# Performance work log

Hardware: AMD Instinct MI355X
Metric: run time of the kernel (lower is better)

Reference implementation:

```python
import jax, jax.numpy as jnp
import numpy as np

N_NODES = 100000   # users + items
EMB_DIM = 64
N_EDGES = 3200000  # avg degree 32
N_LAYERS = 3


def setup_inputs() -> dict:
    key = jax.random.key(0)
    k1, k2, k3, k4 = jax.random.split(key, 4)
    emb = jax.random.normal(k1, (N_NODES, EMB_DIM), dtype=jnp.float32)
    rows = jax.random.randint(k2, (N_EDGES,), 0, N_NODES, dtype=jnp.int32)
    cols = jax.random.randint(k3, (N_EDGES,), 0, N_NODES, dtype=jnp.int32)
    vals = jax.random.uniform(k4, (N_EDGES,), dtype=jnp.float32)
    return {"ItemAndUserEmebddings": emb, "adj_rows": rows,
            "adj_cols": cols, "adj_vals": vals}


def _spmm(rows, cols, vals, x):
    # (sparse A) @ x : gather source rows, scale by edge value, scatter-add to dest
    msgs = vals[:, None] * x[cols]                      # [E, d]
    return jax.ops.segment_sum(msgs, rows, num_segments=x.shape[0])


def reference(ItemAndUserEmebddings, adj_rows, adj_cols, adj_vals):
    all_emb = ItemAndUserEmebddings
    embeddings_list = [all_emb]
    for _ in range(N_LAYERS):
        all_emb = _spmm(adj_rows, adj_cols, adj_vals, all_emb)
        embeddings_list.append(all_emb)
    stacked = jnp.stack(embeddings_list, axis=1)        # [N, L+1, d]
    lightgcn_all_embeddings = jnp.mean(stacked, axis=1)  # [N, d]
    return (lightgcn_all_embeddings, stacked)
```

## Files before the change

kernel.cpp:

```cpp
#include <hip/hip_runtime.h>
#include <hip/hip_fp16.h>

#define N_NODES 100000
#define EMB_DIM 64
#define N_EDGES 3200000
#define N_LAYERS 3

#define SCAN_BLOCK 512
#define N_SCAN_BLOCKS ((N_NODES + SCAN_BLOCK - 1) / SCAN_BLOCK)

#define ABINROWS 256
#define NBINS ((N_NODES + ABINROWS - 1) / ABINROWS)
#define NBINS_P 512
#define ACHUNK 2048
#define AEPT 8
#define NCHUNKS ((N_EDGES + ACHUNK - 1) / ACHUNK)


__device__ __forceinline__ unsigned short f32_to_bf16_rtn(float f) {
    unsigned u = __float_as_uint(f);
    unsigned r = u + 0x7FFFu + ((u >> 16) & 1u);
    return (unsigned short)(r >> 16);
}
__device__ __forceinline__ float bf16_to_f32(unsigned short h) {
    return __uint_as_float(((unsigned)h) << 16);
}


__global__ void count_rows(const int* __restrict__ rows, int* __restrict__ counts) {
    int e = blockIdx.x * blockDim.x + threadIdx.x;
    if (e >= N_EDGES) return;
    atomicAdd(&counts[rows[e]], 1);
}

__global__ void __launch_bounds__(SCAN_BLOCK) scan_phase1(const int* __restrict__ counts,
                                                          int* __restrict__ blockSums) {
    __shared__ int sm[SCAN_BLOCK];
    int idx = blockIdx.x * SCAN_BLOCK + threadIdx.x;
    int v = (idx < N_NODES) ? counts[idx] : 0;
    sm[threadIdx.x] = v;
    __syncthreads();
    for (int off = SCAN_BLOCK / 2; off > 0; off >>= 1) {
        if (threadIdx.x < off) sm[threadIdx.x] += sm[threadIdx.x + off];
        __syncthreads();
    }
    if (threadIdx.x == 0) blockSums[blockIdx.x] = sm[0];
}

__global__ void __launch_bounds__(256) scan_phase2(const int* __restrict__ blockSums,
                                                   int* __restrict__ blockOffs,
                                                   int* __restrict__ row_ptr) {
    __shared__ int sm[256];
    int t = threadIdx.x;
    int v = (t < N_SCAN_BLOCKS) ? blockSums[t] : 0;
    sm[t] = v;
    __syncthreads();
    for (int off = 1; off < 256; off <<= 1) {
        int u = (t >= off) ? sm[t - off] : 0;
        __syncthreads();
        sm[t] += u;
        __syncthreads();
    }
    if (t < N_SCAN_BLOCKS) blockOffs[t] = (t == 0) ? 0 : sm[t - 1];
    if (t == 255) row_ptr[N_NODES] = sm[255];
}

__global__ void __launch_bounds__(SCAN_BLOCK) scan_phase3(const int* __restrict__ counts,
                                                          const int* __restrict__ blockOffs,
                                                          int* __restrict__ row_ptr) {
    __shared__ int sm[SCAN_BLOCK];
    int idx = blockIdx.x * SCAN_BLOCK + threadIdx.x;
    int t = threadIdx.x;
    int v = (idx < N_NODES) ? counts[idx] : 0;
    sm[t] = v;
    __syncthreads();
    for (int off = 1; off < SCAN_BLOCK; off <<= 1) {
        int u = (t >= off) ? sm[t - off] : 0;
        __syncthreads();
        sm[t] += u;
        __syncthreads();
    }
    if (idx < N_NODES) row_ptr[idx] = blockOffs[blockIdx.x] + sm[t] - v;
}


__global__ void __launch_bounds__(256) build_sortA(const int* __restrict__ rows,
                                                   const int* __restrict__ cols,
                                                   const float* __restrict__ vals,
                                                   const int* __restrict__ row_ptr,
                                                   int* __restrict__ bucketFill,
                                                   uint2* __restrict__ records) {
    __shared__ int binCnt[NBINS_P];
    __shared__ int binInc[NBINS_P];
    __shared__ int binCur[NBINS_P];
    __shared__ int binG[NBINS];
    __shared__ uint2 buf[ACHUNK];

    int base = blockIdx.x * ACHUNK;
    int n = N_EDGES - base; if (n > ACHUNK) n = ACHUNK;
    int t = threadIdx.x;

    for (int i = t; i < NBINS_P; i += 256) { binCnt[i] = 0; binCur[i] = 0; }
    __syncthreads();

    int r_[AEPT]; unsigned pk_[AEPT];
#pragma unroll AEPT
    for (int k = 0; k < AEPT; ++k) {
        int i = t + k * 256;
        r_[k] = 0; pk_[k] = 0;
        if (i < n) {
            int e = base + i;
            int r = rows[e];
            unsigned hb = __half_as_ushort(__float2half(vals[e]));
            r_[k] = r;
            pk_[k] = (((unsigned)cols[e]) << 15) | (hb & 0x7FFFu);
            atomicAdd(&binCnt[r >> 8], 1);
        }
    }
    __syncthreads();

    binInc[t] = binCnt[t];
    binInc[t + 256] = binCnt[t + 256];
    __syncthreads();
    for (int off = 1; off < NBINS_P; off <<= 1) {
        int i0 = t, i1 = t + 256;
        int v0 = (i0 >= off) ? binInc[i0 - off] : 0;
        int v1 = (i1 >= off) ? binInc[i1 - off] : 0;
        __syncthreads();
        binInc[i0] += v0;
        binInc[i1] += v1;
        __syncthreads();
    }

#pragma unroll AEPT
    for (int k = 0; k < AEPT; ++k) {
        int i = t + k * 256;
        if (i < n) {
            int b = r_[k] >> 8;
            int slot = (binInc[b] - binCnt[b]) + atomicAdd(&binCur[b], 1);
            buf[slot] = make_uint2((unsigned)r_[k], pk_[k]);
        }
    }
    for (int b = t; b < NBINS; b += 256) {
        int c = binCnt[b];
        if (c > 0) binG[b] = row_ptr[b * ABINROWS] + atomicAdd(&bucketFill[b], c);
    }
    __syncthreads();

    for (int p = t; p < n; p += 256) {
        uint2 rec = buf[p];
        int b = (int)(rec.x >> 8);
        int dst = binG[b] + (p - (binInc[b] - binCnt[b]));
        records[dst] = rec;
    }
}

__global__ void __launch_bounds__(256) build_phaseB(const int* __restrict__ row_ptr,
                                                    const uint2* __restrict__ records,
                                                    unsigned* __restrict__ s_edges) {
    __shared__ int lfill[ABINROWS];
    __shared__ int lrp[ABINROWS];
    int b = blockIdx.x;
    int r0 = b * ABINROWS;
    int r1 = r0 + ABINROWS; if (r1 > N_NODES) r1 = N_NODES;
    int nr = r1 - r0;
    for (int i = threadIdx.x; i < nr; i += 256) { lfill[i] = 0; lrp[i] = row_ptr[r0 + i]; }
    __syncthreads();
    int beg = row_ptr[r0];
    int end = row_ptr[r1];
    for (int i = beg + threadIdx.x; i < end; i += 256) {
        uint2 rec = records[i];
        int lr = (int)rec.x - r0;
        int lp = atomicAdd(&lfill[lr], 1);
        s_edges[lrp[lr] + lp] = rec.y;
    }
}

__global__ void emb_to_bf16(const float* __restrict__ emb, ushort4* __restrict__ mirror) {
    int t = blockIdx.x * blockDim.x + threadIdx.x;
    if (t >= N_NODES * 16) return;
    float4 v = ((const float4*)emb)[t];
    ushort4 o;
    o.x = f32_to_bf16_rtn(v.x); o.y = f32_to_bf16_rtn(v.y);
    o.z = f32_to_bf16_rtn(v.z); o.w = f32_to_bf16_rtn(v.w);
    mirror[t] = o;
}


__device__ __forceinline__ void gacc(float4& acc, unsigned p, int j,
                                     const unsigned short* __restrict__ srcMirror) {
    float v = __half2float(__ushort_as_half((unsigned short)(p & 0x7FFFu)));
    ushort4 m = *(const ushort4*)(srcMirror + (size_t)(p >> 15) * 64 + j * 4);
    acc.x += v * bf16_to_f32(m.x);
    acc.y += v * bf16_to_f32(m.y);
    acc.z += v * bf16_to_f32(m.z);
    acc.w += v * bf16_to_f32(m.w);
}

__device__ __forceinline__ float4 spmm_row_core(int beg, int end, int g, int j, int lane,
                                                const unsigned* __restrict__ s_edges,
                                                const unsigned short* __restrict__ srcMirror) {
    int deg = end - beg;
    unsigned ew = (lane < deg) ? s_edges[beg + lane] : 0u;
    float4 acc = make_float4(0.f, 0.f, 0.f, 0.f);
    int nfull = deg < 64 ? deg : 64;
    for (int kb = 0; kb < nfull; kb += 16) {
        int k0 = kb + g, k1 = kb + g + 4, k2 = kb + g + 8, k3 = kb + g + 12;
        unsigned p0 = __shfl(ew, k0);
        unsigned p1 = __shfl(ew, k1);
        unsigned p2 = __shfl(ew, k2);
        unsigned p3 = __shfl(ew, k3);
        if (k0 < nfull) gacc(acc, p0, j, srcMirror);
        if (k1 < nfull) gacc(acc, p1, j, srcMirror);
        if (k2 < nfull) gacc(acc, p2, j, srcMirror);
        if (k3 < nfull) gacc(acc, p3, j, srcMirror);
    }
    for (int e = beg + 64 + g; e < end; e += 4) {
        unsigned p = s_edges[e];
        gacc(acc, p, j, srcMirror);
    }
    acc.x += __shfl_xor(acc.x, 16); acc.y += __shfl_xor(acc.y, 16);
    acc.z += __shfl_xor(acc.z, 16); acc.w += __shfl_xor(acc.w, 16);
    acc.x += __shfl_xor(acc.x, 32); acc.y += __shfl_xor(acc.y, 32);
    acc.z += __shfl_xor(acc.z, 32); acc.w += __shfl_xor(acc.w, 32);
    return acc;
}

__global__ void __launch_bounds__(256) spmm_gather_bf16_mid(const int* __restrict__ row_ptr,
                                                            const unsigned* __restrict__ s_edges,
                                                            const unsigned short* __restrict__ srcMirror,
                                                            float* __restrict__ dstStacked,
                                                            unsigned short* __restrict__ dstMirror) {
    int wave = (blockIdx.x * blockDim.x + threadIdx.x) >> 6;
    if (wave >= N_NODES) return;
    int lane = threadIdx.x & 63;
    int g = lane >> 4, j = lane & 15;
    float4 acc = spmm_row_core(row_ptr[wave], row_ptr[wave + 1], g, j, lane, s_edges, srcMirror);
    if (lane < 16) {
        *(float4*)(dstStacked + (size_t)wave * 256 + j * 4) = acc;
        ushort4 o;
        o.x = f32_to_bf16_rtn(acc.x); o.y = f32_to_bf16_rtn(acc.y);
        o.z = f32_to_bf16_rtn(acc.z); o.w = f32_to_bf16_rtn(acc.w);
        *(ushort4*)(dstMirror + (size_t)wave * 64 + j * 4) = o;
    }
}

__global__ void __launch_bounds__(256) spmm_gather_bf16_last(const int* __restrict__ row_ptr,
                                                             const unsigned* __restrict__ s_edges,
                                                             const unsigned short* __restrict__ srcMirror,
                                                             const float* __restrict__ emb,
                                                             float* __restrict__ stacked,
                                                             float* __restrict__ meanOut) {
    int wave = (blockIdx.x * blockDim.x + threadIdx.x) >> 6;
    if (wave >= N_NODES) return;
    int lane = threadIdx.x & 63;
    int g = lane >> 4, j = lane & 15;
    float4 acc = spmm_row_core(row_ptr[wave], row_ptr[wave + 1], g, j, lane, s_edges, srcMirror);
    if (lane < 16) {
        float4* base = (float4*)stacked + (size_t)wave * 64;
        float4 a = ((const float4*)emb)[wave * 16 + j];
        float4 b = base[16 + j];
        float4 c = base[32 + j];
        base[j] = a;
        base[48 + j] = acc;
        float4 s;
        s.x = 0.25f * (a.x + b.x + c.x + acc.x);
        s.y = 0.25f * (a.y + b.y + c.y + acc.y);
        s.z = 0.25f * (a.z + b.z + c.z + acc.z);
        s.w = 0.25f * (a.w + b.w + c.w + acc.w);
        ((float4*)meanOut)[wave * 16 + j] = s;
    }
}

__global__ void mean_layers(const float* __restrict__ emb,
                            float* __restrict__ stacked,
                            float* __restrict__ meanOut) {
    int t = blockIdx.x * blockDim.x + threadIdx.x;
    if (t >= N_NODES * 16) return;
    int n = t >> 4;
    int j = t & 15;
    float4* base = (float4*)stacked + (size_t)n * 64;
    float4 a = ((const float4*)emb)[t];
    float4 b = base[16 + j];
    float4 c = base[32 + j];
    float4 d = base[48 + j];
    base[j] = a;
    float4 s;
    s.x = 0.25f * (a.x + b.x + c.x + d.x);
    s.y = 0.25f * (a.y + b.y + c.y + d.y);
    s.z = 0.25f * (a.z + b.z + c.z + d.z);
    s.w = 0.25f * (a.w + b.w + c.w + d.w);
    ((float4*)meanOut)[t] = s;
}


__global__ void scatter_edges_int2(const int* __restrict__ rows, const int* __restrict__ cols,
                                   const float* __restrict__ vals,
                                   const int* __restrict__ row_ptr, int* __restrict__ fill,
                                   int2* __restrict__ s_colval) {
    int e = blockIdx.x * blockDim.x + threadIdx.x;
    if (e >= N_EDGES) return;
    int r = rows[e];
    int pos = row_ptr[r] + atomicAdd(&fill[r], 1);
    int2 p; p.x = cols[e]; p.y = __float_as_int(vals[e]);
    s_colval[pos] = p;
}

__global__ void __launch_bounds__(256) spmm_gather_f32(const int* __restrict__ row_ptr,
                                                       const int2* __restrict__ s_colval,
                                                       const float* __restrict__ src, int srcStride,
                                                       float* __restrict__ dst) {
    int wave = (blockIdx.x * blockDim.x + threadIdx.x) >> 6;
    if (wave >= N_NODES) return;
    int lane = threadIdx.x & 63;
    int g = lane >> 4, j = lane & 15;
    int beg = row_ptr[wave], end = row_ptr[wave + 1];
    float4 acc = make_float4(0.f, 0.f, 0.f, 0.f);
    int e = beg + g;
    for (; e + 4 < end; e += 8) {
        int2 p0 = s_colval[e], p1 = s_colval[e + 4];
        float v0 = __int_as_float(p0.y), v1 = __int_as_float(p1.y);
        float4 m0 = *(const float4*)(src + (size_t)p0.x * srcStride + j * 4);
        float4 m1 = *(const float4*)(src + (size_t)p1.x * srcStride + j * 4);
        acc.x += v0 * m0.x + v1 * m1.x; acc.y += v0 * m0.y + v1 * m1.y;
        acc.z += v0 * m0.z + v1 * m1.z; acc.w += v0 * m0.w + v1 * m1.w;
    }
    for (; e < end; e += 4) {
        int2 p = s_colval[e];
        float v = __int_as_float(p.y);
        float4 m = *(const float4*)(src + (size_t)p.x * srcStride + j * 4);
        acc.x += v * m.x; acc.y += v * m.y; acc.z += v * m.z; acc.w += v * m.w;
    }
    acc.x += __shfl_xor(acc.x, 16); acc.y += __shfl_xor(acc.y, 16);
    acc.z += __shfl_xor(acc.z, 16); acc.w += __shfl_xor(acc.w, 16);
    acc.x += __shfl_xor(acc.x, 32); acc.y += __shfl_xor(acc.y, 32);
    acc.z += __shfl_xor(acc.z, 32); acc.w += __shfl_xor(acc.w, 32);
    if (lane < 16)
        *(float4*)(dst + (size_t)wave * 256 + j * 4) = acc;
}


__global__ void init_stacked_full(const float* __restrict__ emb, float* __restrict__ stacked) {
    int t = blockIdx.x * blockDim.x + threadIdx.x;
    if (t >= N_NODES * 64) return;
    int n = t >> 6, j = t & 63;
    float4 v = (j < 16) ? ((const float4*)emb)[n * 16 + j] : make_float4(0.f, 0.f, 0.f, 0.f);
    ((float4*)stacked)[n * 64 + j] = v;
}

__global__ void spmm_atomic(const int* __restrict__ rows, const int* __restrict__ cols,
                            const float* __restrict__ vals, float* __restrict__ stacked,
                            int lprev) {
    int t = blockIdx.x * blockDim.x + threadIdx.x;
    int e = t >> 4, j = t & 15;
    if (e >= N_EDGES) return;
    int r = rows[e], c = cols[e];
    float v = vals[e];
    const float4* src = (const float4*)(stacked + (size_t)c * 256 + lprev * 64);
    float4 m = src[j];
    float* dst = stacked + (size_t)r * 256 + (lprev + 1) * 64 + j * 4;
    atomicAdd(dst + 0, v * m.x); atomicAdd(dst + 1, v * m.y);
    atomicAdd(dst + 2, v * m.z); atomicAdd(dst + 3, v * m.w);
}

__global__ void mean_layers_plain(const float* __restrict__ stacked, float* __restrict__ meanOut) {
    int t = blockIdx.x * blockDim.x + threadIdx.x;
    if (t >= N_NODES * 16) return;
    int n = t >> 4, j = t & 15;
    const float4* base = (const float4*)(stacked + (size_t)n * 256);
    float4 a = base[j], b = base[16 + j], c = base[32 + j], d = base[48 + j];
    float4 s;
    s.x = 0.25f * (a.x + b.x + c.x + d.x);
    s.y = 0.25f * (a.y + b.y + c.y + d.y);
    s.z = 0.25f * (a.z + b.z + c.z + d.z);
    s.w = 0.25f * (a.w + b.w + c.w + d.w);
    ((float4*)meanOut)[t] = s;
}

extern "C" void kernel_launch(void* const* d_in, const int* in_sizes, int n_in,
                              void* d_out, int out_size, void* d_ws, size_t ws_size,
                              hipStream_t stream) {
    const float* emb  = (const float*)d_in[0];
    const int*   rows = (const int*)d_in[1];
    const int*   cols = (const int*)d_in[2];
    const float* vals = (const float*)d_in[3];

    float* meanOut = (float*)d_out;
    float* stacked = (float*)d_out + (size_t)N_NODES * EMB_DIM;

    const size_t headInts = (size_t)(N_NODES * 2 + 1 + 2 * N_SCAN_BLOCKS);
    size_t need_bf16 = headInts * sizeof(int) + 64
                     + (size_t)N_EDGES * sizeof(unsigned)
                     + 2 * (size_t)N_NODES * EMB_DIM * sizeof(unsigned short);
    size_t need_f32  = headInts * sizeof(int) + 64 + (size_t)N_EDGES * sizeof(int2);

    if (ws_size >= need_bf16) {
        char* w = (char*)d_ws;
        int* counts    = (int*)w;  w += (size_t)N_NODES * sizeof(int);
        int* row_ptr   = (int*)w;  w += (size_t)(N_NODES + 1) * sizeof(int);
        int* blockSums = (int*)w;  w += (size_t)N_SCAN_BLOCKS * sizeof(int);
        int* blockOffs = (int*)w;  w += (size_t)N_SCAN_BLOCKS * sizeof(int);
        w = (char*)(((uintptr_t)w + 15) & ~(uintptr_t)15);
        unsigned* s_edges = (unsigned*)w;  w += (size_t)N_EDGES * sizeof(unsigned);
        unsigned short* mirrorA = (unsigned short*)w;  w += (size_t)N_NODES * EMB_DIM * sizeof(unsigned short);
        unsigned short* mirrorB = (unsigned short*)w;
        uint2* records = (uint2*)mirrorA;

        hipMemsetAsync(counts, 0, (size_t)N_NODES * sizeof(int), stream);
        {
            int block = 256, grid = (N_EDGES + block - 1) / block;
            count_rows<<<grid, block, 0, stream>>>(rows, counts);
        }
        scan_phase1<<<N_SCAN_BLOCKS, SCAN_BLOCK, 0, stream>>>(counts, blockSums);
        scan_phase2<<<1, 256, 0, stream>>>(blockSums, blockOffs, row_ptr);
        scan_phase3<<<N_SCAN_BLOCKS, SCAN_BLOCK, 0, stream>>>(counts, blockOffs, row_ptr);
        int* bucketFill = counts;
        hipMemsetAsync(bucketFill, 0, (size_t)NBINS * sizeof(int), stream);
        build_sortA<<<NCHUNKS, 256, 0, stream>>>(rows, cols, vals, row_ptr, bucketFill, records);
        build_phaseB<<<NBINS, 256, 0, stream>>>(row_ptr, records, s_edges);
        {
            int total = N_NODES * 16;
            int block = 256, grid = (total + block - 1) / block;
            emb_to_bf16<<<grid, block, 0, stream>>>(emb, (ushort4*)mirrorA);
        }
        {
            long long threads = (long long)N_NODES * 64;
            int block = 256;
            int grid = (int)((threads + block - 1) / block);
            spmm_gather_bf16_mid<<<grid, block, 0, stream>>>(row_ptr, s_edges, mirrorA, stacked + 1 * 64, mirrorB);
            spmm_gather_bf16_mid<<<grid, block, 0, stream>>>(row_ptr, s_edges, mirrorB, stacked + 2 * 64, mirrorA);
            spmm_gather_bf16_last<<<grid, block, 0, stream>>>(row_ptr, s_edges, mirrorA, emb, stacked, meanOut);
        }
    } else if (ws_size >= need_f32) {
        char* w = (char*)d_ws;
        int* counts    = (int*)w;  w += (size_t)N_NODES * sizeof(int);
        int* row_ptr   = (int*)w;  w += (size_t)(N_NODES + 1) * sizeof(int);
        int* blockSums = (int*)w;  w += (size_t)N_SCAN_BLOCKS * sizeof(int);
        int* blockOffs = (int*)w;  w += (size_t)N_SCAN_BLOCKS * sizeof(int);
        w = (char*)(((uintptr_t)w + 15) & ~(uintptr_t)15);
        int2* s_colval = (int2*)w;

        hipMemsetAsync(counts, 0, (size_t)N_NODES * sizeof(int), stream);
        {
            int block = 256, grid = (N_EDGES + block - 1) / block;
            count_rows<<<grid, block, 0, stream>>>(rows, counts);
        }
        scan_phase1<<<N_SCAN_BLOCKS, SCAN_BLOCK, 0, stream>>>(counts, blockSums);
        scan_phase2<<<1, 256, 0, stream>>>(blockSums, blockOffs, row_ptr);
        scan_phase3<<<N_SCAN_BLOCKS, SCAN_BLOCK, 0, stream>>>(counts, blockOffs, row_ptr);
        hipMemsetAsync(counts, 0, (size_t)N_NODES * sizeof(int), stream);
        {
            int block = 256, grid = (N_EDGES + block - 1) / block;
            scatter_edges_int2<<<grid, block, 0, stream>>>(rows, cols, vals, row_ptr, counts, s_colval);
        }
        {
            long long threads = (long long)N_NODES * 64;
            int block = 256;
            int grid = (int)((threads + block - 1) / block);
            spmm_gather_f32<<<grid, block, 0, stream>>>(row_ptr, s_colval, emb, 64, stacked + 1 * 64);
            spmm_gather_f32<<<grid, block, 0, stream>>>(row_ptr, s_colval, stacked + 1 * 64, 256, stacked + 2 * 64);
            spmm_gather_f32<<<grid, block, 0, stream>>>(row_ptr, s_colval, stacked + 2 * 64, 256, stacked + 3 * 64);
        }
        {
            int total = N_NODES * 16;
            int block = 256, grid = (total + block - 1) / block;
            mean_layers<<<grid, block, 0, stream>>>(emb, stacked, meanOut);
        }
    } else {
        {
            int total = N_NODES * 64;
            int block = 256, grid = (total + block - 1) / block;
            init_stacked_full<<<grid, block, 0, stream>>>(emb, stacked);
        }
        {
            long long total = (long long)N_EDGES * 16;
            int block = 256, grid = (int)((total + block - 1) / block);
            for (int l = 0; l < N_LAYERS; ++l)
                spmm_atomic<<<grid, block, 0, stream>>>(rows, cols, vals, stacked, l);
        }
        {
            int total = N_NODES * 16;
            int block = 256, grid = (total + block - 1) / block;
            mean_layers_plain<<<grid, block, 0, stream>>>(stacked, meanOut);
        }
    }
}
```

Before: 650.0 us.

## Build CSR row pointers from coarse bin histogram instead of per-row count+scan

```diff
diff --git a/kernel.cpp b/kernel.cpp
--- a/kernel.cpp
+++ b/kernel.cpp
@@ -15,6 +15,8 @@
 #define ACHUNK 2048
 #define AEPT 8
 #define NCHUNKS ((N_EDGES + ACHUNK - 1) / ACHUNK)
+#define BCHUNK 4096
+#define NBCHUNKS ((N_EDGES + BCHUNK - 1) / BCHUNK)
 
 
 __device__ __forceinline__ unsigned short f32_to_bf16_rtn(float f) {
@@ -24,6 +26,40 @@
 }
 __device__ __forceinline__ float bf16_to_f32(unsigned short h) {
     return __uint_as_float(((unsigned)h) << 16);
+}
+
+
+__global__ void __launch_bounds__(256) bin_count(const int* __restrict__ rows,
+                                                 int* __restrict__ binCounts) {
+    __shared__ int h[NBINS];
+    int t = threadIdx.x;
+    for (int i = t; i < NBINS; i += 256) h[i] = 0;
+    __syncthreads();
+    int base = blockIdx.x * BCHUNK;
+    int n = N_EDGES - base; if (n > BCHUNK) n = BCHUNK;
+    for (int i = t; i < n; i += 256) atomicAdd(&h[rows[base + i] >> 8], 1);
+    __syncthreads();
+    for (int i = t; i < NBINS; i += 256) {
+        int c = h[i];
+        if (c) atomicAdd(&binCounts[i], c);
+    }
+}
+
+__global__ void __launch_bounds__(512) bin_scan(const int* __restrict__ binCounts,
+                                                int* __restrict__ binPtr) {
+    __shared__ int sm[512];
+    int t = threadIdx.x;
+    int v = (t < NBINS) ? binCounts[t] : 0;
+    sm[t] = v;
+    __syncthreads();
+    for (int off = 1; off < 512; off <<= 1) {
+        int u = (t >= off) ? sm[t - off] : 0;
+        __syncthreads();
+        sm[t] += u;
+        __syncthreads();
+    }
+    if (t < NBINS) binPtr[t + 1] = sm[t];
+    if (t == 0) binPtr[0] = 0;
 }
 
 
@@ -87,7 +123,7 @@
 __global__ void __launch_bounds__(256) build_sortA(const int* __restrict__ rows,
                                                    const int* __restrict__ cols,
                                                    const float* __restrict__ vals,
-                                                   const int* __restrict__ row_ptr,
+                                                   const int* __restrict__ binPtr,
                                                    int* __restrict__ bucketFill,
                                                    uint2* __restrict__ records) {
     __shared__ int binCnt[NBINS_P];
@@ -143,7 +179,7 @@
     }
     for (int b = t; b < NBINS; b += 256) {
         int c = binCnt[b];
-        if (c > 0) binG[b] = row_ptr[b * ABINROWS] + atomicAdd(&bucketFill[b], c);
+        if (c > 0) binG[b] = binPtr[b] + atomicAdd(&bucketFill[b], c);
     }
     __syncthreads();
 
@@ -155,20 +191,41 @@
     }
 }
 
-__global__ void __launch_bounds__(256) build_phaseB(const int* __restrict__ row_ptr,
+__global__ void __launch_bounds__(256) build_phaseB(const int* __restrict__ binPtr,
                                                     const uint2* __restrict__ records,
-                                                    unsigned* __restrict__ s_edges) {
+                                                    unsigned* __restrict__ s_edges,
+                                                    int* __restrict__ row_ptr) {
+    __shared__ int lcnt[ABINROWS];
+    __shared__ int linc[ABINROWS];
+    __shared__ int lrp[ABINROWS];
     __shared__ int lfill[ABINROWS];
-    __shared__ int lrp[ABINROWS];
     int b = blockIdx.x;
+    int t = threadIdx.x;
     int r0 = b * ABINROWS;
     int r1 = r0 + ABINROWS; if (r1 > N_NODES) r1 = N_NODES;
     int nr = r1 - r0;
-    for (int i = threadIdx.x; i < nr; i += 256) { lfill[i] = 0; lrp[i] = row_ptr[r0 + i]; }
-    __syncthreads();
-    int beg = row_ptr[r0];
-    int end = row_ptr[r1];
-    for (int i = beg + threadIdx.x; i < end; i += 256) {
+    int beg = binPtr[b];
+    int end = binPtr[b + 1];
+
+    lcnt[t] = 0; lfill[t] = 0;
+    __syncthreads();
+    for (int i = beg + t; i < end; i += 256) {
+        atomicAdd(&lcnt[(int)records[i].x - r0], 1);
+    }
+    __syncthreads();
+    linc[t] = lcnt[t];
+    __syncthreads();
+    for (int off = 1; off < 256; off <<= 1) {
+        int u = (t >= off) ? linc[t - off] : 0;
+        __syncthreads();
+        linc[t] += u;
+        __syncthreads();
+    }
+    lrp[t] = beg + linc[t] - lcnt[t];
+    if (t < nr) row_ptr[r0 + t] = lrp[t];
+    if (t == 0) row_ptr[r0 + nr] = end;
+    __syncthreads();
+    for (int i = beg + t; i < end; i += 256) {
         uint2 rec = records[i];
         int lr = (int)rec.x - r0;
         int lp = atomicAdd(&lfill[lr], 1);
@@ -405,19 +462,15 @@
         unsigned short* mirrorA = (unsigned short*)w;  w += (size_t)N_NODES * EMB_DIM * sizeof(unsigned short);
         unsigned short* mirrorB = (unsigned short*)w;
         uint2* records = (uint2*)mirrorA;
-
-        hipMemsetAsync(counts, 0, (size_t)N_NODES * sizeof(int), stream);
-        {
-            int block = 256, grid = (N_EDGES + block - 1) / block;
-            count_rows<<<grid, block, 0, stream>>>(rows, counts);
-        }
-        scan_phase1<<<N_SCAN_BLOCKS, SCAN_BLOCK, 0, stream>>>(counts, blockSums);
-        scan_phase2<<<1, 256, 0, stream>>>(blockSums, blockOffs, row_ptr);
-        scan_phase3<<<N_SCAN_BLOCKS, SCAN_BLOCK, 0, stream>>>(counts, blockOffs, row_ptr);
-        int* bucketFill = counts;
-        hipMemsetAsync(bucketFill, 0, (size_t)NBINS * sizeof(int), stream);
-        build_sortA<<<NCHUNKS, 256, 0, stream>>>(rows, cols, vals, row_ptr, bucketFill, records);
-        build_phaseB<<<NBINS, 256, 0, stream>>>(row_ptr, records, s_edges);
+        int* binCounts  = counts;
+        int* bucketFill = counts + NBINS;
+        int* binPtr     = counts + 2 * NBINS;
+
+        hipMemsetAsync(counts, 0, (size_t)(2 * NBINS) * sizeof(int), stream);
+        bin_count<<<NBCHUNKS, 256, 0, stream>>>(rows, binCounts);
+        bin_scan<<<1, 512, 0, stream>>>(binCounts, binPtr);
+        build_sortA<<<NCHUNKS, 256, 0, stream>>>(rows, cols, vals, binPtr, bucketFill, records);
+        build_phaseB<<<NBINS, 256, 0, stream>>>(binPtr, records, s_edges, row_ptr);
         {
             int total = N_NODES * 16;
             int block = 256, grid = (total + block - 1) / block;
```

New measurement: 572.6 us. 11.9% less time.
